# Optimization experiments

Hardware: AMD Instinct MI355X
Metric: run time of the kernel (lower is better)

The kernel has to match this reference:

```python
import jax, jax.numpy as jnp
import numpy as np

S = 1024   # spkr_num
U = 128    # utt_num
D = 64     # feature dim (hardcoded in original via .view(..., 64))
MARGIN = 0.5
EPS = 1e-07


def _inter_indices():
    # Replicates: temp_centroids = cat(S * [centroids]); n = S+1;
    # inter_centroids = cat_i temp_centroids[i*n+1 : i*n+n]  (last block truncates to empty)
    # temp_centroids[t] == centroids[t % S]. Total kept elements = S*(S-1).
    n = S + 1
    t = np.concatenate([np.arange(i * n + 1, min(i * n + n, S * S)) for i in range(S)])
    cent_idx = (t % S).astype(np.int32)                      # [S*(S-1)] centroid index per pair
    spk_idx = np.repeat(np.arange(S, dtype=np.int32), S - 1)  # maxd_x row j -> speaker j // (S-1)
    return jnp.asarray(spk_idx), jnp.asarray(cent_idx)

SPK_IDX, CENT_IDX = _inter_indices()


def setup_inputs() -> dict:
    key = jax.random.key(0)
    x = jax.random.normal(key, (S, U, D), dtype=jnp.float32)
    return {"x": x}


def reference(x):
    # Per-speaker centroids, L2-normalized (torch F.normalize eps=1e-12)
    centroids = jnp.mean(x, axis=1)                                   # [S, D]
    norm = jnp.maximum(jnp.linalg.norm(centroids, axis=1, keepdims=True), 1e-12)
    centroids = centroids / norm

    # Intra: angular distance of every utterance to its own (normalized) centroid.
    # NOTE: x itself is NOT normalized in the original -- faithful.
    intra_cos = jnp.einsum('sud,sd->su', x, centroids)                # [S, U]
    intra = jnp.arccos(jnp.clip(intra_cos, -1.0 + EPS, 1.0 - EPS))
    intra_d = jnp.max(intra, axis=1)                                  # [S]
    intra_idx = jnp.argmax(intra, axis=1)                             # [S]

    # Hardest utterance per speaker
    xf = x.reshape(S * U, D)
    sel = xf[intra_idx + jnp.arange(S) * U]                           # [S, D]

    # Inter: dot of hardest utterance vs all centroids as one GEMM, then
    # gather the exact pair pattern the original builds via tiling/slicing.
    dots = sel @ centroids.T                                          # [S, S]
    inter_cos = dots[SPK_IDX, CENT_IDX]                               # [S*(S-1)]
    inter = jnp.arccos(jnp.clip(inter_cos, -1.0 + EPS, 1.0 - EPS)).reshape(S, S - 1)
    inter_d = jnp.min(inter, axis=1)                                  # [S]

    return jnp.sum(jnp.maximum(MARGIN + intra_d - inter_d, 0.0))
```

## Files before the change

### kernel.cpp

```cpp
#include <hip/hip_runtime.h>
#include <hip/hip_bf16.h>

#define S 1024
#define U 128
#define D 64
#define EPSC 1e-7f

__global__ __launch_bounds__(256) void k1_centroid_intra(
    const float* __restrict__ x, float* __restrict__ cent_g,
    float* __restrict__ sel_g, float* __restrict__ intra_g)
{
    __shared__ float xs[U * D];
    __shared__ float part[4 * D];
    __shared__ float cent[D];
    __shared__ float red[U];

    const int s = blockIdx.x;
    const int tid = threadIdx.x;

    const float4* __restrict__ xv = (const float4*)(x + (size_t)s * U * D);
    float4* xsv = (float4*)xs;
#pragma unroll
    for (int k = 0; k < 8; ++k) xsv[k * 256 + tid] = xv[k * 256 + tid];
    __syncthreads();

    const int d = tid & 63, g = tid >> 6;
    float acc = 0.f;
    for (int u = g; u < U; u += 4) acc += xs[u * D + d];
    part[g * D + d] = acc;
    __syncthreads();

    if (tid < D) {
        float cm = (part[tid] + part[D + tid] + part[2 * D + tid] + part[3 * D + tid]) * (1.0f / U);
        float sq = cm * cm;
#pragma unroll
        for (int m = 1; m < 64; m <<= 1) sq += __shfl_xor(sq, m, 64);
        float nrm = fmaxf(sqrtf(sq), 1e-12f);
        float c = cm / nrm;
        cent[tid] = c;
        cent_g[s * D + tid] = c;
    }
    __syncthreads();

    if (tid < U) {
        const int u = tid;
        const int off = u & 63;
        float a = 0.f;
#pragma unroll
        for (int k = 0; k < D; ++k) {
            int dd = (k + off) & 63;
            a = fmaf(xs[u * D + dd], cent[dd], a);
        }
        red[u] = fminf(fmaxf(a, -1.0f + EPSC), 1.0f - EPSC);
    }
    __syncthreads();

    if (tid < 64) {
        float v0 = red[tid], v1 = red[tid + 64];
        float mv = fminf(v0, v1);
#pragma unroll
        for (int m = 1; m < 64; m <<= 1) mv = fminf(mv, __shfl_xor(mv, m, 64));
        int idx = (v0 == mv) ? tid : ((v1 == mv) ? (tid + 64) : (1 << 30));
#pragma unroll
        for (int m = 1; m < 64; m <<= 1) idx = min(idx, __shfl_xor(idx, m, 64));
        sel_g[s * D + tid] = xs[idx * D + tid];
        if (tid == 0) intra_g[s] = acosf(mv);
    }
}

__global__ __launch_bounds__(256) void k2_inter(
    const float* __restrict__ cent_g, const float* __restrict__ sel_g,
    const float* __restrict__ intra_g, float* __restrict__ terms)
{
    const int R = 8;
    __shared__ float sels[R * D];
    __shared__ float cc[64 * D];

    const int tid = threadIdx.x;
    const int s0 = blockIdx.x * R;

    if (tid < 128) ((float4*)sels)[tid] = ((const float4*)(sel_g + s0 * D))[tid];

    const int tl = tid & 63;
    const int r0 = tid >> 6;
    float mx0 = -1e30f, mx1 = -1e30f;

    for (int c = 0; c < S / 64; ++c) {
        __syncthreads();
        const float4* __restrict__ cv = (const float4*)(cent_g + c * 64 * D);
        float4* ccv = (float4*)cc;
#pragma unroll
        for (int k = 0; k < 4; ++k) ccv[k * 256 + tid] = cv[k * 256 + tid];
        __syncthreads();

        const int t = c * 64 + tl;
        float a0 = 0.f, a1 = 0.f;
#pragma unroll
        for (int k = 0; k < D; ++k) {
            int dd = (k + tl) & 63;
            float cd = cc[tl * D + dd];
            a0 = fmaf(sels[r0 * D + dd], cd, a0);
            a1 = fmaf(sels[(r0 + 4) * D + dd], cd, a1);
        }
        if (t != s0 + r0) mx0 = fmaxf(mx0, a0);
        if (t != s0 + r0 + 4) mx1 = fmaxf(mx1, a1);
    }

#pragma unroll
    for (int m = 1; m < 64; m <<= 1) {
        mx0 = fmaxf(mx0, __shfl_xor(mx0, m, 64));
        mx1 = fmaxf(mx1, __shfl_xor(mx1, m, 64));
    }
    if (tl == 0) {
        int s = s0 + r0;
        float ic = fminf(fmaxf(mx0, -1.0f + EPSC), 1.0f - EPSC);
        terms[s] = fmaxf(0.5f + intra_g[s] - acosf(ic), 0.0f);
        s = s0 + r0 + 4;
        ic = fminf(fmaxf(mx1, -1.0f + EPSC), 1.0f - EPSC);
        terms[s] = fmaxf(0.5f + intra_g[s] - acosf(ic), 0.0f);
    }
}

__global__ __launch_bounds__(256) void k3_sum(
    const float* __restrict__ terms, float* __restrict__ out)
{
    __shared__ float sred[4];
    const int tid = threadIdx.x;
    float a = 0.f;
    for (int i = tid; i < S; i += 256) a += terms[i];
#pragma unroll
    for (int m = 1; m < 64; m <<= 1) a += __shfl_xor(a, m, 64);
    if ((tid & 63) == 0) sred[tid >> 6] = a;
    __syncthreads();
    if (tid == 0) out[0] = sred[0] + sred[1] + sred[2] + sred[3];
}

extern "C" void kernel_launch(void* const* d_in, const int* in_sizes, int n_in,
                              void* d_out, int out_size, void* d_ws, size_t ws_size,
                              hipStream_t stream) {
    const float* x = (const float*)d_in[0];
    float* out = (float*)d_out;
    float* ws = (float*)d_ws;

    float* cent  = ws;
    float* sel   = ws + S * D;
    float* intra = ws + 2 * S * D;
    float* terms = ws + 2 * S * D + S;

    k1_centroid_intra<<<S, 256, 0, stream>>>(x, cent, sel, intra);
    k2_inter<<<S / 8, 256, 0, stream>>>(cent, sel, intra, terms);
    k3_sum<<<1, 256, 0, stream>>>(terms, out);
}
```

Baseline: 97.71 us.

## Fuse inter-distance and final sum with last-block reduction, read centroids directly

Merges the inter-speaker kernel and the final sum kernel into one kernel: each block writes a partial sum, and the last block to finish, found with an atomic counter that the first kernel resets, does the final reduction. The inter kernel no longer stages centroid tiles through shared memory. Each thread now reads whole centroid rows as float4 from global/L2 and dots them against 4 selected rows, with 256 blocks of 4 speakers instead of 128 blocks of 8. This removes one kernel launch and the shared-memory staging barriers, in exchange for uncoalesced per-thread row reads and atomic/fence overhead.

```diff
diff --git a/kernel.cpp b/kernel.cpp
--- a/kernel.cpp
+++ b/kernel.cpp
@@ -8,7 +8,8 @@
 
 __global__ __launch_bounds__(256) void k1_centroid_intra(
     const float* __restrict__ x, float* __restrict__ cent_g,
-    float* __restrict__ sel_g, float* __restrict__ intra_g)
+    float* __restrict__ sel_g, float* __restrict__ intra_g,
+    int* __restrict__ counter)
 {
     __shared__ float xs[U * D];
     __shared__ float part[4 * D];
@@ -17,6 +18,8 @@
 
     const int s = blockIdx.x;
     const int tid = threadIdx.x;
+
+    if (s == 0 && tid == 0) counter[0] = 0;
 
     const float4* __restrict__ xv = (const float4*)(x + (size_t)s * U * D);
     float4* xsv = (float4*)xs;
@@ -68,71 +71,85 @@
     }
 }
 
-__global__ __launch_bounds__(256) void k2_inter(
+__global__ __launch_bounds__(256) void k2_inter_sum(
     const float* __restrict__ cent_g, const float* __restrict__ sel_g,
-    const float* __restrict__ intra_g, float* __restrict__ terms)
+    const float* __restrict__ intra_g, float* __restrict__ partials,
+    int* __restrict__ counter, float* __restrict__ out)
 {
-    const int R = 8;
-    __shared__ float sels[R * D];
-    __shared__ float cc[64 * D];
+    __shared__ float4 sels4[4 * 16];
+    __shared__ float wred[4][4];
+    __shared__ float sred[4];
+    __shared__ int lastflag;
 
     const int tid = threadIdx.x;
-    const int s0 = blockIdx.x * R;
+    const int s0 = blockIdx.x * 4;
 
-    if (tid < 128) ((float4*)sels)[tid] = ((const float4*)(sel_g + s0 * D))[tid];
+    if (tid < 64) sels4[tid] = ((const float4*)(sel_g + (size_t)s0 * D))[tid];
+    __syncthreads();
 
-    const int tl = tid & 63;
-    const int r0 = tid >> 6;
-    float mx0 = -1e30f, mx1 = -1e30f;
+    float mx0 = -1e30f, mx1 = -1e30f, mx2 = -1e30f, mx3 = -1e30f;
 
-    for (int c = 0; c < S / 64; ++c) {
-        __syncthreads();
-        const float4* __restrict__ cv = (const float4*)(cent_g + c * 64 * D);
-        float4* ccv = (float4*)cc;
 #pragma unroll
-        for (int k = 0; k < 4; ++k) ccv[k * 256 + tid] = cv[k * 256 + tid];
-        __syncthreads();
-
-        const int t = c * 64 + tl;
-        float a0 = 0.f, a1 = 0.f;
+    for (int i = 0; i < 4; ++i) {
+        const int t = i * 256 + tid;
+        const float4* __restrict__ cp = (const float4*)(cent_g + (size_t)t * D);
+        float a0 = 0.f, a1 = 0.f, a2 = 0.f, a3 = 0.f;
 #pragma unroll
-        for (int k = 0; k < D; ++k) {
-            int dd = (k + tl) & 63;
-            float cd = cc[tl * D + dd];
-            a0 = fmaf(sels[r0 * D + dd], cd, a0);
-            a1 = fmaf(sels[(r0 + 4) * D + dd], cd, a1);
+        for (int k = 0; k < 16; ++k) {
+            const float4 c = cp[k];
+            const float4 r0 = sels4[k];
+            const float4 r1 = sels4[16 + k];
+            const float4 r2 = sels4[32 + k];
+            const float4 r3 = sels4[48 + k];
+            a0 = fmaf(c.x, r0.x, fmaf(c.y, r0.y, fmaf(c.z, r0.z, fmaf(c.w, r0.w, a0))));
+            a1 = fmaf(c.x, r1.x, fmaf(c.y, r1.y, fmaf(c.z, r1.z, fmaf(c.w, r1.w, a1))));
+            a2 = fmaf(c.x, r2.x, fmaf(c.y, r2.y, fmaf(c.z, r2.z, fmaf(c.w, r2.w, a2))));
+            a3 = fmaf(c.x, r3.x, fmaf(c.y, r3.y, fmaf(c.z, r3.z, fmaf(c.w, r3.w, a3))));
         }
-        if (t != s0 + r0) mx0 = fmaxf(mx0, a0);
-        if (t != s0 + r0 + 4) mx1 = fmaxf(mx1, a1);
+        if (t != s0)     mx0 = fmaxf(mx0, a0);
+        if (t != s0 + 1) mx1 = fmaxf(mx1, a1);
+        if (t != s0 + 2) mx2 = fmaxf(mx2, a2);
+        if (t != s0 + 3) mx3 = fmaxf(mx3, a3);
     }
 
 #pragma unroll
     for (int m = 1; m < 64; m <<= 1) {
         mx0 = fmaxf(mx0, __shfl_xor(mx0, m, 64));
         mx1 = fmaxf(mx1, __shfl_xor(mx1, m, 64));
+        mx2 = fmaxf(mx2, __shfl_xor(mx2, m, 64));
+        mx3 = fmaxf(mx3, __shfl_xor(mx3, m, 64));
     }
-    if (tl == 0) {
-        int s = s0 + r0;
-        float ic = fminf(fmaxf(mx0, -1.0f + EPSC), 1.0f - EPSC);
-        terms[s] = fmaxf(0.5f + intra_g[s] - acosf(ic), 0.0f);
-        s = s0 + r0 + 4;
-        ic = fminf(fmaxf(mx1, -1.0f + EPSC), 1.0f - EPSC);
-        terms[s] = fmaxf(0.5f + intra_g[s] - acosf(ic), 0.0f);
+    const int w = tid >> 6;
+    if ((tid & 63) == 0) {
+        wred[w][0] = mx0; wred[w][1] = mx1; wred[w][2] = mx2; wred[w][3] = mx3;
     }
-}
+    __syncthreads();
 
-__global__ __launch_bounds__(256) void k3_sum(
-    const float* __restrict__ terms, float* __restrict__ out)
-{
-    __shared__ float sred[4];
-    const int tid = threadIdx.x;
-    float a = 0.f;
-    for (int i = tid; i < S; i += 256) a += terms[i];
+    if (tid < 4) {
+        float m = fmaxf(fmaxf(wred[0][tid], wred[1][tid]),
+                        fmaxf(wred[2][tid], wred[3][tid]));
+        float ic = fminf(fmaxf(m, -1.0f + EPSC), 1.0f - EPSC);
+        wred[0][tid] = fmaxf(0.5f + intra_g[s0 + tid] - acosf(ic), 0.0f);
+    }
+    __syncthreads();
+
+    if (tid == 0) {
+        partials[blockIdx.x] = wred[0][0] + wred[0][1] + wred[0][2] + wred[0][3];
+        __threadfence();
+        int old = atomicAdd(counter, 1);
+        lastflag = (old == (int)gridDim.x - 1) ? 1 : 0;
+    }
+    __syncthreads();
+
+    if (lastflag) {
+        __threadfence();
+        float a = partials[tid];
 #pragma unroll
-    for (int m = 1; m < 64; m <<= 1) a += __shfl_xor(a, m, 64);
-    if ((tid & 63) == 0) sred[tid >> 6] = a;
-    __syncthreads();
-    if (tid == 0) out[0] = sred[0] + sred[1] + sred[2] + sred[3];
+        for (int m = 1; m < 64; m <<= 1) a += __shfl_xor(a, m, 64);
+        if ((tid & 63) == 0) sred[tid >> 6] = a;
+        __syncthreads();
+        if (tid == 0) out[0] = sred[0] + sred[1] + sred[2] + sred[3];
+    }
 }
 
 extern "C" void kernel_launch(void* const* d_in, const int* in_sizes, int n_in,
@@ -142,12 +159,12 @@
     float* out = (float*)d_out;
     float* ws = (float*)d_ws;
 
-    float* cent  = ws;
-    float* sel   = ws + S * D;
-    float* intra = ws + 2 * S * D;
-    float* terms = ws + 2 * S * D + S;
+    float* cent     = ws;
+    float* sel      = ws + S * D;
+    float* intra    = ws + 2 * S * D;
+    float* partials = ws + 2 * S * D + S;
+    int*   counter  = (int*)(ws + 2 * S * D + S + 256);
 
-    k1_centroid_intra<<<S, 256, 0, stream>>>(x, cent, sel, intra);
-    k2_inter<<<S / 8, 256, 0, stream>>>(cent, sel, intra, terms);
-    k3_sum<<<1, 256, 0, stream>>>(terms, out);
+    k1_centroid_intra<<<S, 256, 0, stream>>>(x, cent, sel, intra, counter);
+    k2_inter_sum<<<S / 4, 256, 0, stream>>>(cent, sel, intra, partials, counter, out);
 }
```

Measured after the change: 97.18 us. About the same (-0.5%).
